# Optimization experiments

Hardware: AMD Instinct MI355X
Metric: run time of the kernel (lower is better)

## Reference

```python
import jax, jax.numpy as jnp
import numpy as np

N_QUBITS = 8
DEPTH = 2
INPUT_DIM = 128
HIDDEN_DIM = 256
SEQ_LEN = 64
BATCH = 128
DIM = 2 ** N_QUBITS


def _rx(t):
    c = jnp.cos(0.5 * t).astype(jnp.complex64)
    s = (-1j * jnp.sin(0.5 * t)).astype(jnp.complex64)
    return jnp.stack([jnp.stack([c, s], -1), jnp.stack([s, c], -1)], -2)


def _ry(t):
    c = jnp.cos(0.5 * t).astype(jnp.complex64)
    s = jnp.sin(0.5 * t).astype(jnp.complex64)
    return jnp.stack([jnp.stack([c, -s], -1), jnp.stack([s, c], -1)], -2)


def _rz(t):
    e0 = jnp.exp(-0.5j * t).astype(jnp.complex64)
    e1 = jnp.exp(0.5j * t).astype(jnp.complex64)
    z = jnp.zeros_like(e0)
    return jnp.stack([jnp.stack([e0, z], -1), jnp.stack([z, e1], -1)], -2)


def _apply_1q(state, U, q):
    # state: (B, 2**n) complex; U: (2,2) shared or (B,2,2) per-sample
    b = state.shape[0]
    s = state.reshape(b, 2 ** q, 2, -1)
    if U.ndim == 2:
        s = jnp.einsum('ij,bljr->blir', U, s)
    else:
        s = jnp.einsum('bij,bljr->blir', U, s)
    return s.reshape(b, DIM)


def _apply_cnot(state, c, t):
    b = state.shape[0]
    s = state.reshape((b,) + (2,) * N_QUBITS)
    ac, at = 1 + c, 1 + t
    s0 = jnp.take(s, 0, axis=ac)
    s1 = jnp.take(s, 1, axis=ac)
    at2 = at - 1 if at > ac else at  # target axis shifts after slicing control axis
    s1 = jnp.flip(s1, axis=at2)
    s = jnp.stack([s0, s1], axis=ac)
    return s.reshape(b, DIM)


def _quantum_gate(x, params):
    # x: (B, n_qubits) data angles; params: (n_qubits, depth, 3) RX/RY/RZ angles
    b = x.shape[0]
    state = jnp.zeros((b, DIM), jnp.complex64).at[:, 0].set(1.0)
    for q in range(N_QUBITS):
        state = _apply_1q(state, _rx(x[:, q]), q)
    for d in range(DEPTH):
        for q in range(N_QUBITS):
            state = _apply_1q(state, _rx(params[q, d, 0]), q)
            state = _apply_1q(state, _ry(params[q, d, 1]), q)
            state = _apply_1q(state, _rz(params[q, d, 2]), q)
        for q in range(N_QUBITS - 1):
            state = _apply_cnot(state, q, q + 1)
        state = _apply_cnot(state, N_QUBITS - 1, 0)
    probs = state.real ** 2 + state.imag ** 2
    outs = []
    for q in range(N_QUBITS):  # <Z_q> = P(q=0) - P(q=1)
        p = probs.reshape(b, 2 ** q, 2, -1)
        outs.append(p[:, :, 0, :].sum((1, 2)) - p[:, :, 1, :].sum((1, 2)))
    return jnp.stack(outs, axis=1)


def _qlstm(inputs, Wf, bf, qf, Uf, cf, Wi, bi, qi, Ui, ci, Wg, bg, qg, Ug, cg, Wo, bo, qo, Uo, co):
    B = inputs.shape[1]
    h0 = jnp.zeros((B, HIDDEN_DIM), inputs.dtype)
    c0 = jnp.zeros((B, HIDDEN_DIM), inputs.dtype)

    def step(carry, x):
        hx, cx = carry
        comb = jnp.concatenate([x, hx], axis=1)

        def gate(W, b_, qp, U, c_):
            return _quantum_gate(comb @ W.T + b_, qp) @ U.T + c_

        f = jax.nn.sigmoid(gate(Wf, bf, qf, Uf, cf))
        i = jax.nn.sigmoid(gate(Wi, bi, qi, Ui, ci))
        g = jnp.tanh(gate(Wg, bg, qg, Ug, cg))
        o = jax.nn.sigmoid(gate(Wo, bo, qo, Uo, co))
        cx2 = f * cx + i * g
        hx2 = o * jnp.tanh(cx2)
        return (hx2, cx2), hx2

    (hx, cx), stacked = jax.lax.scan(step, (h0, c0), inputs)
    return stacked, hx, cx


def setup_inputs() -> dict:
    key = jax.random.key(0)
    ks = jax.random.split(key, 16)
    d = INPUT_DIM + HIDDEN_DIM
    inp = {"inputs": jax.random.normal(ks[0], (SEQ_LEN, BATCH, INPUT_DIM), jnp.float32)}
    k = 1
    for n in ("f", "i", "g", "o"):
        inp["W" + n] = jax.random.normal(ks[k], (N_QUBITS, d), jnp.float32) * 0.05; k += 1
        inp["b" + n] = jnp.zeros((N_QUBITS,), jnp.float32)
        inp["q" + n] = jax.random.normal(ks[k], (N_QUBITS, DEPTH, 3), jnp.float32) * 0.1; k += 1
        inp["U" + n] = jax.random.normal(ks[k], (HIDDEN_DIM, N_QUBITS), jnp.float32) * 0.05; k += 1
        inp["c" + n] = jnp.zeros((HIDDEN_DIM,), jnp.float32)
    return inp


def reference(inputs, Wf, bf, qf, Uf, cf, Wi, bi, qi, Ui, ci, Wg, bg, qg, Ug, cg, Wo, bo, qo, Uo, co):
    stacked, hx, cx = _qlstm(inputs, Wf, bf, qf, Uf, cf, Wi, bi, qi, Ui, ci,
                             Wg, bg, qg, Ug, cg, Wo, bo, qo, Uo, co)
    return stacked, (hx, cx)
```

## Files before the change

### kernel.cpp

```cpp
#include <hip/hip_runtime.h>
#include <math.h>

#define BB   128
#define TT   64
#define IND  128
#define HID  256
#define CD   384

typedef float v2f __attribute__((ext_vector_type(2)));

struct C2 { float x, y; };
__device__ __forceinline__ C2 cmul(C2 a, C2 b) { return {a.x*b.x - a.y*b.y, a.x*b.y + a.y*b.x}; }
__device__ __forceinline__ C2 cadd(C2 a, C2 b) { return {a.x + b.x, a.y + b.y}; }
__device__ __forceinline__ C2 csub(C2 a, C2 b) { return {a.x - b.x, a.y - b.y}; }
__device__ __forceinline__ C2 conjc(C2 a) { return {a.x, -a.y}; }

__device__ __forceinline__ v2f pk(float a, float b) { v2f r; r.x = a; r.y = b; return r; }
__device__ __forceinline__ v2f swp(v2f v) { return __builtin_shufflevector(v, v, 1, 0); }

struct Args {
    const float* x;
    const float* W[4];
    const float* bb[4];
    const float* qp[4];
    const float* Uo[4];
    const float* cb[4];
    float* out;
};

template<int CTRL>
__device__ __forceinline__ int dppmv(int v) {
    return __builtin_amdgcn_update_dpp(v, v, CTRL, 0xF, 0xF, false);
}

template<int M>
__device__ __forceinline__ float lx(float v) {
    int i = __float_as_int(v);
    if constexpr (M == 1)
        return __int_as_float(dppmv<0xB1>(i));
    else if constexpr (M == 2)
        return __int_as_float(dppmv<0x4E>(i));
    else if constexpr (M == 4) {
        int a = dppmv<0x104>(i);
        int b = dppmv<0x114>(i);
        return __int_as_float((threadIdx.x & 4) ? b : a);
    } else if constexpr (M == 8)
        return __int_as_float(dppmv<0x128>(i));
    else if constexpr (M == 16) {
#if __has_builtin(__builtin_amdgcn_permlane16_swap)
        auto r = __builtin_amdgcn_permlane16_swap(i, i, false, false);
        return __int_as_float((threadIdx.x & 16) ? r[0] : r[1]);
#else
        return __int_as_float(__builtin_amdgcn_ds_swizzle(i, 0x401F));
#endif
    } else {
#if __has_builtin(__builtin_amdgcn_permlane32_swap)
        auto r = __builtin_amdgcn_permlane32_swap(i, i, false, false);
        return __int_as_float((threadIdx.x & 32) ? r[0] : r[1]);
#else
        return __shfl_xor(v, 32);
#endif
    }
}
template<int M>
__device__ __forceinline__ v2f lx2(v2f v) {
    return pk(lx<M>(v.x), lx<M>(v.y));
}

__device__ __forceinline__ float rfl(float v) {
    return __int_as_float(__builtin_amdgcn_readfirstlane(__float_as_int(v)));
}
__device__ __forceinline__ float bcast_lane(float v, int srclane) {
    return __int_as_float(__builtin_amdgcn_readlane(__float_as_int(v), srclane));
}
__device__ __forceinline__ float sigm(float x) {
    return __builtin_amdgcn_rcpf(1.f + __expf(-x));
}
__device__ __forceinline__ float tanh_fast(float x) {
    float e = __expf(2.f * x);
    return 1.f - 2.f * __builtin_amdgcn_rcpf(e + 1.f);
}
__device__ __forceinline__ float sgnx(float v, unsigned m) {
    return __int_as_float(__float_as_int(v) ^ (int)m);
}

template<int M>
__device__ __forceinline__ void gate_lane_pk(v2f& xe01, v2f& xi01, v2f& xe23, v2f& xi23,
                                             float u0, float u1, float u2, float u3) {
    v2f px0 = lx2<M>(xe01), py0 = lx2<M>(xi01);
    v2f px2 = lx2<M>(xe23), py2 = lx2<M>(xi23);
    v2f ne0 = u0*xe01 - u1*xi01 + u2*px0 - u3*py0;
    v2f ni0 = u0*xi01 + u1*xe01 + u2*py0 + u3*px0;
    v2f ne2 = u0*xe23 - u1*xi23 + u2*px2 - u3*py2;
    v2f ni2 = u0*xi23 + u1*xe23 + u2*py2 + u3*px2;
    xe01 = ne0; xi01 = ni0; xe23 = ne2; xi23 = ni2;
}

__global__ __launch_bounds__(256, 1) void qlstm_kernel(Args a) {
    const int b    = blockIdx.x;
    const int tid  = threadIdx.x;
    const int lane = tid & 63;
    const int wv   = tid >> 6;

    __shared__ float Ax[TT][32];
    __shared__ __align__(16) float hH[16][HID];
    __shared__ __align__(16) float4 uab[4][2][8];
    __shared__ __align__(16) float expL[32];

    const int a_ang = tid >> 3, p = tid & 7;
    const int g_ang = a_ang >> 3, q_ang = a_ang & 7;
    v2f whr2[8][2];
    {
        const float* Wg = a.W[g_ang] + q_ang * CD + IND;
#pragma unroll
        for (int k = 0; k < 8; ++k) {
            int base = p * 32 + ((4 * (k + p)) & 31);
            whr2[k][0] = pk(Wg[base + 0], Wg[base + 1]);
            whr2[k][1] = pk(Wg[base + 2], Wg[base + 3]);
        }
    }
    v2f ur2a[8], ur2b[8], cb2a, cb2b;
#pragma unroll
    for (int k = 0; k < 8; ++k) {
        ur2a[k] = pk(a.Uo[0][tid * 8 + k], a.Uo[1][tid * 8 + k]);
        ur2b[k] = pk(a.Uo[2][tid * 8 + k], a.Uo[3][tid * 8 + k]);
    }
    cb2a = pk(a.cb[0][tid], a.cb[1][tid]);
    cb2b = pk(a.cb[2][tid], a.cb[3][tid]);

    if (tid < 64) {
        int g = tid >> 4, d = (tid >> 3) & 1, q = tid & 7;
        const float* qp = a.qp[g] + q * 6 + d * 3;
        float s0, c0, s1, c1, s2, c2;
        sincosf(0.5f * qp[0], &s0, &c0);
        sincosf(0.5f * qp[1], &s1, &c1);
        sincosf(0.5f * qp[2], &s2, &c2);
        C2 aX{c0, 0.f}, bX{0.f, -s0};
        C2 aY{c1, 0.f}, bY{-s1, 0.f};
        C2 aB = csub(cmul(aY, aX), cmul(bY, conjc(bX)));
        C2 bB = cadd(cmul(aY, bX), cmul(bY, conjc(aX)));
        C2 aZ{c2, -s2};
        C2 al = cmul(aZ, aB), be = cmul(aZ, bB);
        uab[g][d][q] = make_float4(al.x, al.y, be.x, be.y);
    }

    for (int rep = 0; rep < 8; ++rep) {
        int idx = rep * 256 + tid;
        int t = idx >> 5, aa = idx & 31;
        int gg = aa >> 3, qq = aa & 7;
        const float4* w4 = (const float4*)(a.W[gg] + qq * CD);
        const float4* x4 = (const float4*)(a.x + (size_t)(t * BB + b) * IND);
        float acc = a.bb[gg][qq];
        for (int e = 0; e < IND / 4; ++e) {
            float4 xv = x4[e], wvv = w4[e];
            acc += xv.x * wvv.x + xv.y * wvv.y + xv.z * wvv.z + xv.w * wvv.w;
        }
        Ax[t][aa] = acc;
    }

    hH[15][tid] = 0.f;
    float creg = 0.f, h = 0.f;
    __syncthreads();

    v2f pA[8], pB[8], pC[8], pD[8];
#pragma unroll
    for (int q = 0; q < 8; ++q) {
        float4 u = uab[wv][0][q];
        float ax = rfl(u.x), ay = rfl(u.y), bx = rfl(u.z), by = rfl(u.w);
        pA[q] = pk(ax, -bx);
        pB[q] = pk(by, -ay);
        pC[q] = pk(ay, by);
        pD[q] = pk(-bx, -ax);
    }
    float gA[6][4];
#pragma unroll
    for (int qi = 0; qi < 6; ++qi) {
        float4 u = uab[wv][1][qi + 2];
        bool bit = (lane >> (5 - qi)) & 1;
        gA[qi][0] = u.x;
        gA[qi][1] = bit ? -u.y : u.y;
        gA[qi][2] = bit ? -u.z : u.z;
        gA[qi][3] = u.w;
    }
    float q0ax, q0ay, q0bx, q0by;
    float q1ax, q1by;
    v2f q1aym, q1ayp, q1bxm;
    {
        float4 u0 = uab[wv][1][0], u1 = uab[wv][1][1];
        q0ax = rfl(u0.x); q0ay = rfl(u0.y); q0bx = rfl(u0.z); q0by = rfl(u0.w);
        q1ax = rfl(u1.x); q1by = rfl(u1.w);
        float ay = rfl(u1.y), bx = rfl(u1.z);
        q1aym = pk(-ay, ay);
        q1ayp = pk(ay, -ay);
        q1bxm = pk(bx, -bx);
    }

    const bool st3 = ((lane >> 4) ^ (lane >> 5)) & 1;
    const bool st4 = ((lane >> 3) ^ (lane >> 4)) & 1;
    const bool st5 = ((lane >> 2) ^ (lane >> 3)) & 1;
    const bool st6 = ((lane >> 1) ^ (lane >> 2)) & 1;
    const bool st7 = (lane ^ (lane >> 1)) & 1;
    const bool sp2 = (lane >> 5) & 1;
    const bool sp7 = lane & 1;

    unsigned sg0, sg2, sg3, sg4, sg5, sg6, sg7;
    {
        auto par31 = [](int v) -> unsigned { return (unsigned)(__popc(v) & 1) << 31; };
        sg0 = par31(lane & 63);
        sg2 = par31(lane & 32);
        sg3 = par31(lane & 48);
        sg4 = par31(lane & 56);
        sg5 = par31(lane & 60);
        sg6 = par31(lane & 62);
        sg7 = sg0;
    }

    for (int t = 0; t < TT; ++t) {
        const int rowPrev = (t + 15) & 15;
        const float* hrow = hH[rowPrev];
        v2f acc2 = pk(0.f, 0.f);
#pragma unroll
        for (int k = 0; k < 8; ++k) {
            int base = p * 32 + ((4 * (k + p)) & 31);
            const float4 hv = *reinterpret_cast<const float4*>(&hrow[base]);
            acc2 = acc2 + pk(hv.x, hv.y) * whr2[k][0] + pk(hv.z, hv.w) * whr2[k][1];
        }
        float acc = acc2.x + acc2.y;
        acc += lx<1>(acc);
        acc += lx<2>(acc);
        acc += lx<4>(acc);
        float ang = 0.5f * (acc + Ax[t][a_ang]);
        float cA = __cosf(ang), sA = __sinf(ang);
        float cs_c[8], cs_s[8];
#pragma unroll
        for (int q = 0; q < 8; ++q) {
            cs_c[q] = bcast_lane(cA, q * 8);
            cs_s[q] = bcast_lane(sA, q * 8);
        }

        v2f Vx[8], Vy[8];
#pragma unroll
        for (int q = 0; q < 8; ++q) {
            Vx[q] = pA[q] * cs_c[q] + pB[q] * cs_s[q];
            Vy[q] = pC[q] * cs_c[q] + pD[q] * cs_s[q];
        }

        v2f xe01, xi01, xe23, xi23;
        {
            C2 f3{ st3 ? Vx[3].y : Vx[3].x, st3 ? Vy[3].y : Vy[3].x };
            C2 f4{ st4 ? Vx[4].y : Vx[4].x, st4 ? Vy[4].y : Vy[4].x };
            C2 f5{ st5 ? Vx[5].y : Vx[5].x, st5 ? Vy[5].y : Vy[5].x };
            C2 f6{ st6 ? Vx[6].y : Vx[6].x, st6 ? Vy[6].y : Vy[6].x };
            C2 f7{ st7 ? Vx[7].y : Vx[7].x, st7 ? Vy[7].y : Vy[7].x };
            C2 c5 = cmul(cmul(cmul(f3, f4), cmul(f5, f6)), f7);
            v2f f2re = sp2 ? swp(Vx[2]) : Vx[2];
            v2f f2im = sp2 ? swp(Vy[2]) : Vy[2];
            v2f c2re = c5.x * f2re - c5.y * f2im;
            v2f c2im = c5.x * f2im + c5.y * f2re;
            v2f f1re = sp7 ? swp(Vx[1]) : Vx[1];
            v2f f1im = sp7 ? swp(Vy[1]) : Vy[1];
            float f0ax = sp7 ? Vx[0].y : Vx[0].x, f0ay = sp7 ? Vy[0].y : Vy[0].x;
            float f0bx = sp7 ? Vx[0].x : Vx[0].y, f0by = sp7 ? Vy[0].x : Vy[0].y;
            v2f uure = f1re * f0ax - f1im * f0ay;
            v2f uuim = f1re * f0ay + f1im * f0ax;
            v2f s1re = swp(f1re), s1im = swp(f1im);
            v2f wwre = s1re * f0bx - s1im * f0by;
            v2f wwim = s1re * f0by + s1im * f0bx;
            xe01 = c2re * uure - c2im * uuim;
            xi01 = c2re * uuim + c2im * uure;
            xe23 = c2re * wwre - c2im * wwim;
            xi23 = c2re * wwim + c2im * wwre;
        }

        {
            v2f ne01 = q0ax*xe01 - q0ay*xi01 + q0bx*xe23 - q0by*xi23;
            v2f ni01 = q0ax*xi01 + q0ay*xe01 + q0bx*xi23 + q0by*xe23;
            v2f ne23 = -q0bx*xe01 - q0by*xi01 + q0ax*xe23 + q0ay*xi23;
            v2f ni23 = -q0bx*xi01 + q0by*xe01 + q0ax*xi23 - q0ay*xe23;
            xe01 = ne01; xi01 = ni01; xe23 = ne23; xi23 = ni23;
        }
        {
            v2f se01 = swp(xe01), si01 = swp(xi01);
            v2f se23 = swp(xe23), si23 = swp(xi23);
            v2f ne01 = q1ax*xe01 + q1aym*xi01 + q1bxm*se01 - q1by*si01;
            v2f ni01 = q1ax*xi01 + q1ayp*xe01 + q1bxm*si01 + q1by*se01;
            v2f ne23 = q1ax*xe23 + q1aym*xi23 + q1bxm*se23 - q1by*si23;
            v2f ni23 = q1ax*xi23 + q1ayp*xe23 + q1bxm*si23 + q1by*se23;
            xe01 = ne01; xi01 = ni01; xe23 = ne23; xi23 = ni23;
        }
        gate_lane_pk<32>(xe01, xi01, xe23, xi23, gA[0][0], gA[0][1], gA[0][2], gA[0][3]);
        gate_lane_pk<16>(xe01, xi01, xe23, xi23, gA[1][0], gA[1][1], gA[1][2], gA[1][3]);
        gate_lane_pk< 8>(xe01, xi01, xe23, xi23, gA[2][0], gA[2][1], gA[2][2], gA[2][3]);
        gate_lane_pk< 4>(xe01, xi01, xe23, xi23, gA[3][0], gA[3][1], gA[3][2], gA[3][3]);
        gate_lane_pk< 2>(xe01, xi01, xe23, xi23, gA[4][0], gA[4][1], gA[4][2], gA[4][3]);
        gate_lane_pk< 1>(xe01, xi01, xe23, xi23, gA[5][0], gA[5][1], gA[5][2], gA[5][3]);

        v2f pr01 = xe01 * xe01 + xi01 * xi01;
        v2f pr23 = xe23 * xe23 + xi23 * xi23;
        float pr0 = pr01.x, pr1 = pr01.y, pr2 = pr23.x, pr3 = pr23.y;
        float Bc = pr0 - pr1 + pr2 - pr3;
        float Dc = pr0 - pr1 - pr2 + pr3;
        v2f zA = pk(sgnx(Bc, sg0), Dc);
        v2f zB = pk(sgnx(Dc, sg2), sgnx(Dc, sg3));
        v2f zC = pk(sgnx(Dc, sg4), sgnx(Dc, sg5));
        v2f zD = pk(sgnx(Dc, sg6), sgnx(Dc, sg7));
        zA = zA + lx2<1>(zA);  zB = zB + lx2<1>(zB);  zC = zC + lx2<1>(zC);  zD = zD + lx2<1>(zD);
        zA = zA + lx2<2>(zA);  zB = zB + lx2<2>(zB);  zC = zC + lx2<2>(zC);  zD = zD + lx2<2>(zD);
        zA = zA + lx2<4>(zA);  zB = zB + lx2<4>(zB);  zC = zC + lx2<4>(zC);  zD = zD + lx2<4>(zD);
        zA = zA + lx2<8>(zA);  zB = zB + lx2<8>(zB);  zC = zC + lx2<8>(zC);  zD = zD + lx2<8>(zD);
        zA = zA + lx2<16>(zA); zB = zB + lx2<16>(zB); zC = zC + lx2<16>(zC); zD = zD + lx2<16>(zD);
        zA = zA + lx2<32>(zA); zB = zB + lx2<32>(zB); zC = zC + lx2<32>(zC); zD = zD + lx2<32>(zD);
        if (lane == 0) {
            expL[0*4 + wv] = zA.x; expL[1*4 + wv] = zA.y;
            expL[2*4 + wv] = zB.x; expL[3*4 + wv] = zB.y;
            expL[4*4 + wv] = zC.x; expL[5*4 + wv] = zC.y;
            expL[6*4 + wv] = zD.x; expL[7*4 + wv] = zD.y;
        }
        __syncthreads();

        const float4* eL4 = (const float4*)expL;
        v2f og2a = cb2a, og2b = cb2b;
#pragma unroll
        for (int k = 0; k < 8; ++k) {
            float4 e4 = eL4[k];
            og2a = og2a + pk(e4.x, e4.y) * ur2a[k];
            og2b = og2b + pk(e4.z, e4.w) * ur2b[k];
        }
        float fg = sigm(og2a.x);
        float ig = sigm(og2a.y);
        float gg = tanh_fast(og2b.x);
        float oo = sigm(og2b.y);
        creg = fg * creg + ig * gg;
        h = oo * tanh_fast(creg);

        hH[t & 15][tid] = h;
        if ((t & 15) == 15) {
            int t0 = t - 15;
#pragma unroll
            for (int r = 0; r < 16; ++r)
                a.out[(size_t)((t0 + r) * BB + b) * HID + tid] = hH[r][tid];
        }
        __syncthreads();
    }

    a.out[(size_t)TT * BB * HID + (size_t)b * HID + tid] = h;
    a.out[(size_t)TT * BB * HID + (size_t)BB * HID + (size_t)b * HID + tid] = creg;
}

extern "C" void kernel_launch(void* const* d_in, const int* in_sizes, int n_in,
                              void* d_out, int out_size, void* d_ws, size_t ws_size,
                              hipStream_t stream) {
    (void)in_sizes; (void)n_in; (void)out_size; (void)d_ws; (void)ws_size;
    Args ar;
    ar.x = (const float*)d_in[0];
    for (int g = 0; g < 4; ++g) {
        ar.W[g]  = (const float*)d_in[1 + 5 * g];
        ar.bb[g] = (const float*)d_in[2 + 5 * g];
        ar.qp[g] = (const float*)d_in[3 + 5 * g];
        ar.Uo[g] = (const float*)d_in[4 + 5 * g];
        ar.cb[g] = (const float*)d_in[5 + 5 * g];
    }
    ar.out = (float*)d_out;
    qlstm_kernel<<<dim3(BB), dim3(256), 0, stream>>>(ar);
}
```

Before: 131.3 us.

## Process two batch samples per block to interleave independent recurrence chains

Each block now handles two batch elements, running their recurrent matvec, quantum circuit, reductions and LSTM updates side by side in each time step, and the grid shrinks from 128 to 64 blocks. The goal is instruction-level parallelism from two independent dependency chains and amortising the per-step barriers and latency across two samples. In exchange, register pressure roughly doubles for the circuit state, and only 64 of the many compute units are used, so per-block serial work doubles.

```diff
diff --git a/kernel.cpp b/kernel.cpp
--- a/kernel.cpp
+++ b/kernel.cpp
@@ -97,15 +97,15 @@
 }
 
 __global__ __launch_bounds__(256, 1) void qlstm_kernel(Args a) {
-    const int b    = blockIdx.x;
+    const int b0   = blockIdx.x * 2, b1 = b0 + 1;
     const int tid  = threadIdx.x;
     const int lane = tid & 63;
     const int wv   = tid >> 6;
 
-    __shared__ float Ax[TT][32];
-    __shared__ __align__(16) float hH[16][HID];
+    __shared__ float Ax[2][TT][32];
+    __shared__ __align__(16) float hH[2][16][HID];
     __shared__ __align__(16) float4 uab[4][2][8];
-    __shared__ __align__(16) float expL[32];
+    __shared__ __align__(16) float expL[2][32];
 
     const int a_ang = tid >> 3, p = tid & 7;
     const int g_ang = a_ang >> 3, q_ang = a_ang & 7;
@@ -144,22 +144,23 @@
         uab[g][d][q] = make_float4(al.x, al.y, be.x, be.y);
     }
 
-    for (int rep = 0; rep < 8; ++rep) {
+    for (int rep = 0; rep < 16; ++rep) {
         int idx = rep * 256 + tid;
-        int t = idx >> 5, aa = idx & 31;
+        int s = idx >> 11, t = (idx >> 5) & 63, aa = idx & 31;
         int gg = aa >> 3, qq = aa & 7;
         const float4* w4 = (const float4*)(a.W[gg] + qq * CD);
-        const float4* x4 = (const float4*)(a.x + (size_t)(t * BB + b) * IND);
+        const float4* x4 = (const float4*)(a.x + (size_t)(t * BB + b0 + s) * IND);
         float acc = a.bb[gg][qq];
         for (int e = 0; e < IND / 4; ++e) {
             float4 xv = x4[e], wvv = w4[e];
             acc += xv.x * wvv.x + xv.y * wvv.y + xv.z * wvv.z + xv.w * wvv.w;
         }
-        Ax[t][aa] = acc;
-    }
-
-    hH[15][tid] = 0.f;
-    float creg = 0.f, h = 0.f;
+        Ax[s][t][aa] = acc;
+    }
+
+    hH[0][15][tid] = 0.f;
+    hH[1][15][tid] = 0.f;
+    float creg0 = 0.f, h0 = 0.f, creg1 = 0.f, h1 = 0.f;
     __syncthreads();
 
     v2f pA[8], pB[8], pC[8], pD[8];
@@ -182,8 +183,7 @@
         gA[qi][2] = bit ? -u.z : u.z;
         gA[qi][3] = u.w;
     }
-    float q0ax, q0ay, q0bx, q0by;
-    float q1ax, q1by;
+    float q0ax, q0ay, q0bx, q0by, q1ax, q1by;
     v2f q1aym, q1ayp, q1bxm;
     {
         float4 u0 = uab[wv][1][0], u1 = uab[wv][1][1];
@@ -215,37 +215,14 @@
         sg7 = sg0;
     }
 
-    for (int t = 0; t < TT; ++t) {
-        const int rowPrev = (t + 15) & 15;
-        const float* hrow = hH[rowPrev];
-        v2f acc2 = pk(0.f, 0.f);
-#pragma unroll
-        for (int k = 0; k < 8; ++k) {
-            int base = p * 32 + ((4 * (k + p)) & 31);
-            const float4 hv = *reinterpret_cast<const float4*>(&hrow[base]);
-            acc2 = acc2 + pk(hv.x, hv.y) * whr2[k][0] + pk(hv.z, hv.w) * whr2[k][1];
-        }
-        float acc = acc2.x + acc2.y;
-        acc += lx<1>(acc);
-        acc += lx<2>(acc);
-        acc += lx<4>(acc);
-        float ang = 0.5f * (acc + Ax[t][a_ang]);
-        float cA = __cosf(ang), sA = __sinf(ang);
-        float cs_c[8], cs_s[8];
-#pragma unroll
-        for (int q = 0; q < 8; ++q) {
-            cs_c[q] = bcast_lane(cA, q * 8);
-            cs_s[q] = bcast_lane(sA, q * 8);
-        }
-
+    auto run_circuit = [&](const float (&cs_c)[8], const float (&cs_s)[8],
+                           v2f& xe01, v2f& xi01, v2f& xe23, v2f& xi23) {
         v2f Vx[8], Vy[8];
 #pragma unroll
         for (int q = 0; q < 8; ++q) {
             Vx[q] = pA[q] * cs_c[q] + pB[q] * cs_s[q];
             Vy[q] = pC[q] * cs_c[q] + pD[q] * cs_s[q];
         }
-
-        v2f xe01, xi01, xe23, xi23;
         {
             C2 f3{ st3 ? Vx[3].y : Vx[3].x, st3 ? Vy[3].y : Vy[3].x };
             C2 f4{ st4 ? Vx[4].y : Vx[4].x, st4 ? Vy[4].y : Vy[4].x };
@@ -271,7 +248,6 @@
             xe23 = c2re * wwre - c2im * wwim;
             xi23 = c2re * wwim + c2im * wwre;
         }
-
         {
             v2f ne01 = q0ax*xe01 - q0ay*xi01 + q0bx*xe23 - q0by*xi23;
             v2f ni01 = q0ax*xi01 + q0ay*xe01 + q0bx*xi23 + q0by*xe23;
@@ -294,57 +270,131 @@
         gate_lane_pk< 4>(xe01, xi01, xe23, xi23, gA[3][0], gA[3][1], gA[3][2], gA[3][3]);
         gate_lane_pk< 2>(xe01, xi01, xe23, xi23, gA[4][0], gA[4][1], gA[4][2], gA[4][3]);
         gate_lane_pk< 1>(xe01, xi01, xe23, xi23, gA[5][0], gA[5][1], gA[5][2], gA[5][3]);
-
+    };
+
+    auto butterfly = [&](v2f xe01, v2f xi01, v2f xe23, v2f xi23,
+                         v2f& zA, v2f& zB, v2f& zC, v2f& zD) {
         v2f pr01 = xe01 * xe01 + xi01 * xi01;
         v2f pr23 = xe23 * xe23 + xi23 * xi23;
         float pr0 = pr01.x, pr1 = pr01.y, pr2 = pr23.x, pr3 = pr23.y;
         float Bc = pr0 - pr1 + pr2 - pr3;
         float Dc = pr0 - pr1 - pr2 + pr3;
-        v2f zA = pk(sgnx(Bc, sg0), Dc);
-        v2f zB = pk(sgnx(Dc, sg2), sgnx(Dc, sg3));
-        v2f zC = pk(sgnx(Dc, sg4), sgnx(Dc, sg5));
-        v2f zD = pk(sgnx(Dc, sg6), sgnx(Dc, sg7));
+        zA = pk(sgnx(Bc, sg0), Dc);
+        zB = pk(sgnx(Dc, sg2), sgnx(Dc, sg3));
+        zC = pk(sgnx(Dc, sg4), sgnx(Dc, sg5));
+        zD = pk(sgnx(Dc, sg6), sgnx(Dc, sg7));
         zA = zA + lx2<1>(zA);  zB = zB + lx2<1>(zB);  zC = zC + lx2<1>(zC);  zD = zD + lx2<1>(zD);
         zA = zA + lx2<2>(zA);  zB = zB + lx2<2>(zB);  zC = zC + lx2<2>(zC);  zD = zD + lx2<2>(zD);
         zA = zA + lx2<4>(zA);  zB = zB + lx2<4>(zB);  zC = zC + lx2<4>(zC);  zD = zD + lx2<4>(zD);
         zA = zA + lx2<8>(zA);  zB = zB + lx2<8>(zB);  zC = zC + lx2<8>(zC);  zD = zD + lx2<8>(zD);
         zA = zA + lx2<16>(zA); zB = zB + lx2<16>(zB); zC = zC + lx2<16>(zC); zD = zD + lx2<16>(zD);
         zA = zA + lx2<32>(zA); zB = zB + lx2<32>(zB); zC = zC + lx2<32>(zC); zD = zD + lx2<32>(zD);
+    };
+
+    for (int t = 0; t < TT; ++t) {
+        const int rowPrev = (t + 15) & 15;
+        const float* hrow0 = hH[0][rowPrev];
+        const float* hrow1 = hH[1][rowPrev];
+        v2f acc2_0 = pk(0.f, 0.f), acc2_1 = pk(0.f, 0.f);
+#pragma unroll
+        for (int k = 0; k < 8; ++k) {
+            int base = p * 32 + ((4 * (k + p)) & 31);
+            const float4 hv0 = *reinterpret_cast<const float4*>(&hrow0[base]);
+            const float4 hv1 = *reinterpret_cast<const float4*>(&hrow1[base]);
+            acc2_0 = acc2_0 + pk(hv0.x, hv0.y) * whr2[k][0] + pk(hv0.z, hv0.w) * whr2[k][1];
+            acc2_1 = acc2_1 + pk(hv1.x, hv1.y) * whr2[k][0] + pk(hv1.z, hv1.w) * whr2[k][1];
+        }
+        float acc0 = acc2_0.x + acc2_0.y;
+        float acc1 = acc2_1.x + acc2_1.y;
+        acc0 += lx<1>(acc0);  acc1 += lx<1>(acc1);
+        acc0 += lx<2>(acc0);  acc1 += lx<2>(acc1);
+        acc0 += lx<4>(acc0);  acc1 += lx<4>(acc1);
+        float ang0 = 0.5f * (acc0 + Ax[0][t][a_ang]);
+        float ang1 = 0.5f * (acc1 + Ax[1][t][a_ang]);
+        float cA0 = __cosf(ang0), sA0 = __sinf(ang0);
+        float cA1 = __cosf(ang1), sA1 = __sinf(ang1);
+        float cs_c0[8], cs_s0[8], cs_c1[8], cs_s1[8];
+#pragma unroll
+        for (int q = 0; q < 8; ++q) {
+            cs_c0[q] = bcast_lane(cA0, q * 8);
+            cs_s0[q] = bcast_lane(sA0, q * 8);
+            cs_c1[q] = bcast_lane(cA1, q * 8);
+            cs_s1[q] = bcast_lane(sA1, q * 8);
+        }
+
+        v2f xe01_0, xi01_0, xe23_0, xi23_0;
+        v2f xe01_1, xi01_1, xe23_1, xi23_1;
+        run_circuit(cs_c0, cs_s0, xe01_0, xi01_0, xe23_0, xi23_0);
+        run_circuit(cs_c1, cs_s1, xe01_1, xi01_1, xe23_1, xi23_1);
+
+        v2f zA0, zB0, zC0, zD0, zA1, zB1, zC1, zD1;
+        butterfly(xe01_0, xi01_0, xe23_0, xi23_0, zA0, zB0, zC0, zD0);
+        butterfly(xe01_1, xi01_1, xe23_1, xi23_1, zA1, zB1, zC1, zD1);
+
         if (lane == 0) {
-            expL[0*4 + wv] = zA.x; expL[1*4 + wv] = zA.y;
-            expL[2*4 + wv] = zB.x; expL[3*4 + wv] = zB.y;
-            expL[4*4 + wv] = zC.x; expL[5*4 + wv] = zC.y;
-            expL[6*4 + wv] = zD.x; expL[7*4 + wv] = zD.y;
+            expL[0][0*4 + wv] = zA0.x; expL[0][1*4 + wv] = zA0.y;
+            expL[0][2*4 + wv] = zB0.x; expL[0][3*4 + wv] = zB0.y;
+            expL[0][4*4 + wv] = zC0.x; expL[0][5*4 + wv] = zC0.y;
+            expL[0][6*4 + wv] = zD0.x; expL[0][7*4 + wv] = zD0.y;
+        }
+        if (lane == 1) {
+            expL[1][0*4 + wv] = zA1.x; expL[1][1*4 + wv] = zA1.y;
+            expL[1][2*4 + wv] = zB1.x; expL[1][3*4 + wv] = zB1.y;
+            expL[1][4*4 + wv] = zC1.x; expL[1][5*4 + wv] = zC1.y;
+            expL[1][6*4 + wv] = zD1.x; expL[1][7*4 + wv] = zD1.y;
         }
         __syncthreads();
 
-        const float4* eL4 = (const float4*)expL;
-        v2f og2a = cb2a, og2b = cb2b;
-#pragma unroll
-        for (int k = 0; k < 8; ++k) {
-            float4 e4 = eL4[k];
-            og2a = og2a + pk(e4.x, e4.y) * ur2a[k];
-            og2b = og2b + pk(e4.z, e4.w) * ur2b[k];
-        }
-        float fg = sigm(og2a.x);
-        float ig = sigm(og2a.y);
-        float gg = tanh_fast(og2b.x);
-        float oo = sigm(og2b.y);
-        creg = fg * creg + ig * gg;
-        h = oo * tanh_fast(creg);
-
-        hH[t & 15][tid] = h;
+        {
+            const float4* eL4 = (const float4*)expL[0];
+            v2f og2a = cb2a, og2b = cb2b;
+#pragma unroll
+            for (int k = 0; k < 8; ++k) {
+                float4 e4 = eL4[k];
+                og2a = og2a + pk(e4.x, e4.y) * ur2a[k];
+                og2b = og2b + pk(e4.z, e4.w) * ur2b[k];
+            }
+            float fg = sigm(og2a.x);
+            float ig = sigm(og2a.y);
+            float gg = tanh_fast(og2b.x);
+            float oo = sigm(og2b.y);
+            creg0 = fg * creg0 + ig * gg;
+            h0 = oo * tanh_fast(creg0);
+        }
+        {
+            const float4* eL4 = (const float4*)expL[1];
+            v2f og2a = cb2a, og2b = cb2b;
+#pragma unroll
+            for (int k = 0; k < 8; ++k) {
+                float4 e4 = eL4[k];
+                og2a = og2a + pk(e4.x, e4.y) * ur2a[k];
+                og2b = og2b + pk(e4.z, e4.w) * ur2b[k];
+            }
+            float fg = sigm(og2a.x);
+            float ig = sigm(og2a.y);
+            float gg = tanh_fast(og2b.x);
+            float oo = sigm(og2b.y);
+            creg1 = fg * creg1 + ig * gg;
+            h1 = oo * tanh_fast(creg1);
+        }
+
+        hH[0][t & 15][tid] = h0;
+        hH[1][t & 15][tid] = h1;
         if ((t & 15) == 15) {
             int t0 = t - 15;
 #pragma unroll
-            for (int r = 0; r < 16; ++r)
-                a.out[(size_t)((t0 + r) * BB + b) * HID + tid] = hH[r][tid];
+            for (int r = 0; r < 16; ++r) {
+                a.out[(size_t)((t0 + r) * BB + b0) * HID + tid] = hH[0][r][tid];
+                a.out[(size_t)((t0 + r) * BB + b1) * HID + tid] = hH[1][r][tid];
+            }
         }
         __syncthreads();
     }
 
-    a.out[(size_t)TT * BB * HID + (size_t)b * HID + tid] = h;
-    a.out[(size_t)TT * BB * HID + (size_t)BB * HID + (size_t)b * HID + tid] = creg;
+    a.out[(size_t)TT * BB * HID + (size_t)b0 * HID + tid] = h0;
+    a.out[(size_t)TT * BB * HID + (size_t)b1 * HID + tid] = h1;
+    a.out[(size_t)TT * BB * HID + (size_t)BB * HID + (size_t)b0 * HID + tid] = creg0;
+    a.out[(size_t)TT * BB * HID + (size_t)BB * HID + (size_t)b1 * HID + tid] = creg1;
 }
 
 extern "C" void kernel_launch(void* const* d_in, const int* in_sizes, int n_in,
@@ -361,5 +411,5 @@
         ar.cb[g] = (const float*)d_in[5 + 5 * g];
     }
     ar.out = (float*)d_out;
-    qlstm_kernel<<<dim3(BB), dim3(256), 0, stream>>>(ar);
-}
+    qlstm_kernel<<<dim3(BB / 2), dim3(256), 0, stream>>>(ar);
+}
```

Result: slower. 256.3 us (+95.2%).

## Pack two batch samples per 512-thread block to halve block count

Applied to the files above, without the earlier changes.

Each block now handles two batch samples, with 8 waves split into two groups of four, and launches 64 blocks instead of 128. Shared buffers gain a per-sample dimension, and both samples share one __syncthreads per step. The aim is to use fewer CUs and interleave two independent recurrences per CU to hide latency. The cost is that each block-wide barrier now waits for both samples, and the launch bound of 512 threads with 2 blocks per CU may limit registers per thread.

```diff
diff --git a/kernel.cpp b/kernel.cpp
--- a/kernel.cpp
+++ b/kernel.cpp
@@ -96,18 +96,22 @@
     xe01 = ne0; xi01 = ni0; xe23 = ne2; xi23 = ni2;
 }
 
-__global__ __launch_bounds__(256, 1) void qlstm_kernel(Args a) {
-    const int b    = blockIdx.x;
+__global__ __launch_bounds__(512, 2) void qlstm_kernel(Args a) {
+    const int b0   = blockIdx.x * 2;
     const int tid  = threadIdx.x;
     const int lane = tid & 63;
     const int wv   = tid >> 6;
-
-    __shared__ float Ax[TT][32];
-    __shared__ __align__(16) float hH[16][HID];
+    const int g    = wv & 3;
+    const int smp  = wv >> 2;
+    const int l    = tid & 255;
+    const int b    = b0 + smp;
+
+    __shared__ float Ax[2][TT][32];
+    __shared__ __align__(16) float hH[2][16][HID];
     __shared__ __align__(16) float4 uab[4][2][8];
-    __shared__ __align__(16) float expL[32];
-
-    const int a_ang = tid >> 3, p = tid & 7;
+    __shared__ __align__(16) float expL[2][32];
+
+    const int a_ang = l >> 3, p = l & 7;
     const int g_ang = a_ang >> 3, q_ang = a_ang & 7;
     v2f whr2[8][2];
     {
@@ -122,15 +126,15 @@
     v2f ur2a[8], ur2b[8], cb2a, cb2b;
 #pragma unroll
     for (int k = 0; k < 8; ++k) {
-        ur2a[k] = pk(a.Uo[0][tid * 8 + k], a.Uo[1][tid * 8 + k]);
-        ur2b[k] = pk(a.Uo[2][tid * 8 + k], a.Uo[3][tid * 8 + k]);
-    }
-    cb2a = pk(a.cb[0][tid], a.cb[1][tid]);
-    cb2b = pk(a.cb[2][tid], a.cb[3][tid]);
+        ur2a[k] = pk(a.Uo[0][l * 8 + k], a.Uo[1][l * 8 + k]);
+        ur2b[k] = pk(a.Uo[2][l * 8 + k], a.Uo[3][l * 8 + k]);
+    }
+    cb2a = pk(a.cb[0][l], a.cb[1][l]);
+    cb2b = pk(a.cb[2][l], a.cb[3][l]);
 
     if (tid < 64) {
-        int g = tid >> 4, d = (tid >> 3) & 1, q = tid & 7;
-        const float* qp = a.qp[g] + q * 6 + d * 3;
+        int gg = tid >> 4, d = (tid >> 3) & 1, q = tid & 7;
+        const float* qp = a.qp[gg] + q * 6 + d * 3;
         float s0, c0, s1, c1, s2, c2;
         sincosf(0.5f * qp[0], &s0, &c0);
         sincosf(0.5f * qp[1], &s1, &c1);
@@ -141,31 +145,31 @@
         C2 bB = cadd(cmul(aY, bX), cmul(bY, conjc(aX)));
         C2 aZ{c2, -s2};
         C2 al = cmul(aZ, aB), be = cmul(aZ, bB);
-        uab[g][d][q] = make_float4(al.x, al.y, be.x, be.y);
+        uab[gg][d][q] = make_float4(al.x, al.y, be.x, be.y);
     }
 
     for (int rep = 0; rep < 8; ++rep) {
-        int idx = rep * 256 + tid;
-        int t = idx >> 5, aa = idx & 31;
+        int idx = rep * 512 + tid;
+        int s = idx >> 11, t = (idx >> 5) & 63, aa = idx & 31;
         int gg = aa >> 3, qq = aa & 7;
         const float4* w4 = (const float4*)(a.W[gg] + qq * CD);
-        const float4* x4 = (const float4*)(a.x + (size_t)(t * BB + b) * IND);
+        const float4* x4 = (const float4*)(a.x + (size_t)(t * BB + b0 + s) * IND);
         float acc = a.bb[gg][qq];
         for (int e = 0; e < IND / 4; ++e) {
             float4 xv = x4[e], wvv = w4[e];
             acc += xv.x * wvv.x + xv.y * wvv.y + xv.z * wvv.z + xv.w * wvv.w;
         }
-        Ax[t][aa] = acc;
-    }
-
-    hH[15][tid] = 0.f;
+        Ax[s][t][aa] = acc;
+    }
+
+    hH[smp][15][l] = 0.f;
     float creg = 0.f, h = 0.f;
     __syncthreads();
 
     v2f pA[8], pB[8], pC[8], pD[8];
 #pragma unroll
     for (int q = 0; q < 8; ++q) {
-        float4 u = uab[wv][0][q];
+        float4 u = uab[g][0][q];
         float ax = rfl(u.x), ay = rfl(u.y), bx = rfl(u.z), by = rfl(u.w);
         pA[q] = pk(ax, -bx);
         pB[q] = pk(by, -ay);
@@ -175,7 +179,7 @@
     float gA[6][4];
 #pragma unroll
     for (int qi = 0; qi < 6; ++qi) {
-        float4 u = uab[wv][1][qi + 2];
+        float4 u = uab[g][1][qi + 2];
         bool bit = (lane >> (5 - qi)) & 1;
         gA[qi][0] = u.x;
         gA[qi][1] = bit ? -u.y : u.y;
@@ -186,7 +190,7 @@
     float q1ax, q1by;
     v2f q1aym, q1ayp, q1bxm;
     {
-        float4 u0 = uab[wv][1][0], u1 = uab[wv][1][1];
+        float4 u0 = uab[g][1][0], u1 = uab[g][1][1];
         q0ax = rfl(u0.x); q0ay = rfl(u0.y); q0bx = rfl(u0.z); q0by = rfl(u0.w);
         q1ax = rfl(u1.x); q1by = rfl(u1.w);
         float ay = rfl(u1.y), bx = rfl(u1.z);
@@ -217,7 +221,7 @@
 
     for (int t = 0; t < TT; ++t) {
         const int rowPrev = (t + 15) & 15;
-        const float* hrow = hH[rowPrev];
+        const float* hrow = hH[smp][rowPrev];
         v2f acc2 = pk(0.f, 0.f);
 #pragma unroll
         for (int k = 0; k < 8; ++k) {
@@ -229,7 +233,7 @@
         acc += lx<1>(acc);
         acc += lx<2>(acc);
         acc += lx<4>(acc);
-        float ang = 0.5f * (acc + Ax[t][a_ang]);
+        float ang = 0.5f * (acc + Ax[smp][t][a_ang]);
         float cA = __cosf(ang), sA = __sinf(ang);
         float cs_c[8], cs_s[8];
 #pragma unroll
@@ -311,14 +315,14 @@
         zA = zA + lx2<16>(zA); zB = zB + lx2<16>(zB); zC = zC + lx2<16>(zC); zD = zD + lx2<16>(zD);
         zA = zA + lx2<32>(zA); zB = zB + lx2<32>(zB); zC = zC + lx2<32>(zC); zD = zD + lx2<32>(zD);
         if (lane == 0) {
-            expL[0*4 + wv] = zA.x; expL[1*4 + wv] = zA.y;
-            expL[2*4 + wv] = zB.x; expL[3*4 + wv] = zB.y;
-            expL[4*4 + wv] = zC.x; expL[5*4 + wv] = zC.y;
-            expL[6*4 + wv] = zD.x; expL[7*4 + wv] = zD.y;
+            expL[smp][0*4 + g] = zA.x; expL[smp][1*4 + g] = zA.y;
+            expL[smp][2*4 + g] = zB.x; expL[smp][3*4 + g] = zB.y;
+            expL[smp][4*4 + g] = zC.x; expL[smp][5*4 + g] = zC.y;
+            expL[smp][6*4 + g] = zD.x; expL[smp][7*4 + g] = zD.y;
         }
         __syncthreads();
 
-        const float4* eL4 = (const float4*)expL;
+        const float4* eL4 = (const float4*)expL[smp];
         v2f og2a = cb2a, og2b = cb2b;
 #pragma unroll
         for (int k = 0; k < 8; ++k) {
@@ -333,18 +337,18 @@
         creg = fg * creg + ig * gg;
         h = oo * tanh_fast(creg);
 
-        hH[t & 15][tid] = h;
+        hH[smp][t & 15][l] = h;
         if ((t & 15) == 15) {
             int t0 = t - 15;
 #pragma unroll
             for (int r = 0; r < 16; ++r)
-                a.out[(size_t)((t0 + r) * BB + b) * HID + tid] = hH[r][tid];
+                a.out[(size_t)((t0 + r) * BB + b) * HID + l] = hH[smp][r][l];
         }
         __syncthreads();
     }
 
-    a.out[(size_t)TT * BB * HID + (size_t)b * HID + tid] = h;
-    a.out[(size_t)TT * BB * HID + (size_t)BB * HID + (size_t)b * HID + tid] = creg;
+    a.out[(size_t)TT * BB * HID + (size_t)b * HID + l] = h;
+    a.out[(size_t)TT * BB * HID + (size_t)BB * HID + (size_t)b * HID + l] = creg;
 }
 
 extern "C" void kernel_launch(void* const* d_in, const int* in_sizes, int n_in,
@@ -361,5 +365,5 @@
         ar.cb[g] = (const float*)d_in[5 + 5 * g];
     }
     ar.out = (float*)d_out;
-    qlstm_kernel<<<dim3(BB), dim3(256), 0, stream>>>(ar);
-}
+    qlstm_kernel<<<dim3(BB / 2), dim3(512), 0, stream>>>(ar);
+}
```

Measured after the change: 238.5 us. 1.82x slower.
